# Performance work log

Measured on AMD Instinct MI355X. Metric: run time of the kernel, lower is better.

Reference implementation:

```python
import jax, jax.numpy as jnp
import numpy as np

T, B, D, Hd = 512, 64, 1024, 1024
SIGMA = 0.01


def setup_inputs() -> dict:
    key = jax.random.key(0)
    ks = jax.random.split(key, 9)
    inp = {
        "inputs": jax.random.normal(ks[0], (T, B, D), dtype=jnp.float32),
        "H0": jnp.zeros((B, Hd), dtype=jnp.float32),
        "C0": jnp.zeros((B, Hd), dtype=jnp.float32),
    }
    names_x = ["W_xi", "W_xf", "W_xo", "W_xc"]
    names_h = ["W_hi", "W_hf", "W_ho", "W_hc"]
    for i, n in enumerate(names_x):
        inp[n] = jax.random.normal(ks[1 + i], (D, Hd), dtype=jnp.float32) * SIGMA
    for i, n in enumerate(names_h):
        inp[n] = jax.random.normal(ks[5 + i], (Hd, Hd), dtype=jnp.float32) * SIGMA
    for n in ["b_i", "b_f", "b_o", "b_c"]:
        inp[n] = jnp.zeros((Hd,), dtype=jnp.float32)
    return inp


def reference(inputs, H0, C0, W_xi, W_xf, W_xo, W_xc,
              W_hi, W_hf, W_ho, W_hc, b_i, b_f, b_o, b_c):
    # Fuse the 4 input-projection and 4 hidden-projection GEMMs into 2 GEMMs
    # per step (same math as 8 separate matmuls, just concatenated).
    Wx = jnp.concatenate([W_xi, W_xf, W_xo, W_xc], axis=1)   # [D, 4H]
    Wh = jnp.concatenate([W_hi, W_hf, W_ho, W_hc], axis=1)   # [H, 4H]
    b = jnp.concatenate([b_i, b_f, b_o, b_c], axis=0)        # [4H]
    nh = b_i.shape[0]

    def step(carry, X):
        H, C = carry
        gates = X @ Wx + H @ Wh + b                          # [B, 4H]
        i, f, o, g = jnp.split(gates, 4, axis=1)
        I = jax.nn.sigmoid(i)
        F = jax.nn.sigmoid(f)
        O = jax.nn.sigmoid(o)
        C_tilde = jnp.tanh(g)
        C_new = F * C + I * C_tilde
        H_new = O * jnp.tanh(C_new)
        return (H_new, C_new), H_new

    (H_f, C_f), outputs = jax.lax.scan(step, (H0, C0), inputs)  # outputs [T, B, H]
    return outputs, (H_f, C_f)
```

## Files before the change

kernel.cpp:

```cpp
#include <hip/hip_runtime.h>
#include <cstdint>

#define TT 512
#define BB 64
#define DD 1024
#define HH 1024
#define NWG 128

typedef __attribute__((ext_vector_type(8))) __bf16 bf16x8;
typedef __attribute__((ext_vector_type(4))) float f32x4;

#define WS_XQ    0
#define WS_WHB   67108864ULL
#define WS_HQ    83886080ULL
#define WS_FLAGS 151126016ULL
#define FLAGS_BYTES ((TT + 1) * NWG * 4)

__device__ __forceinline__ unsigned short f2bf(float f) {
    unsigned int u = __float_as_uint(f);
    u = (u + 0x7fffu + ((u >> 16) & 1u)) >> 16;
    return (unsigned short)u;
}

__device__ __forceinline__ float sigm(float x) {
    return 1.0f / (1.0f + __expf(-x));
}
__device__ __forceinline__ float tanh_f(float x) {
    float a = fabsf(x);
    float e = __expf(-2.0f * a);
    float t = (1.0f - e) / (1.0f + e);
    return copysignf(t, x);
}

__device__ __forceinline__ unsigned long long pack4bf(float a, float b, float c, float d) {
    return (unsigned long long)f2bf(a)
         | ((unsigned long long)f2bf(b) << 16)
         | ((unsigned long long)f2bf(c) << 32)
         | ((unsigned long long)f2bf(d) << 48);
}

__global__ void cvt_x(const float* __restrict__ X, unsigned short* __restrict__ Xq) {
    int i = blockIdx.x * blockDim.x + threadIdx.x;
    const int n8 = TT * BB * DD / 8;
    if (i >= n8) return;
    const float4* s = (const float4*)X;
    float4 a = s[2 * i], b = s[2 * i + 1];
    union { unsigned short u[8]; uint4 q; } r;
    r.u[0] = f2bf(a.x); r.u[1] = f2bf(a.y); r.u[2] = f2bf(a.z); r.u[3] = f2bf(a.w);
    r.u[4] = f2bf(b.x); r.u[5] = f2bf(b.y); r.u[6] = f2bf(b.z); r.u[7] = f2bf(b.w);
    ((uint4*)Xq)[i] = r.q;
}

__global__ void pack_w(const float* __restrict__ Wxi, const float* __restrict__ Wxf,
                       const float* __restrict__ Wxo, const float* __restrict__ Wxc,
                       const float* __restrict__ Whi, const float* __restrict__ Whf,
                       const float* __restrict__ Who, const float* __restrict__ Whc,
                       unsigned short* __restrict__ WhB) {
    int tid = blockIdx.x * blockDim.x + threadIdx.x;
    int lane = tid & 63;
    int ct   = (tid >> 6) & 1;
    int s    = (tid >> 7) & 15;
    int kq   = (tid >> 11) & 3;
    int wg   = tid >> 13;
    int col  = ct * 16 + (lane & 15);
    int gate = col >> 3;
    int h    = wg * 8 + (col & 7);
    int kb   = kq * 512 + s * 32 + ((lane >> 4) & 3) * 8;

    const float* Wx[4] = {Wxi, Wxf, Wxo, Wxc};
    const float* Wh[4] = {Whi, Whf, Who, Whc};
    const float* W = (kb < 1024) ? (Wx[gate] + (size_t)kb * HH + h)
                                 : (Wh[gate] + (size_t)(kb - 1024) * HH + h);
    union { unsigned short u[8]; uint4 q; } r;
#pragma unroll
    for (int m = 0; m < 8; ++m) r.u[m] = f2bf(W[(size_t)m * HH]);
    *(uint4*)(WhB + (size_t)tid * 8) = r.q;
}

__global__ void __launch_bounds__(512, 2)
lstm_seq(const unsigned short* __restrict__ Xq, const unsigned short* __restrict__ WhB,
         unsigned short* __restrict__ Hq, int* flags,
         const float* __restrict__ H0, const float* __restrict__ C0,
         const float* __restrict__ bi, const float* __restrict__ bfp,
         const float* __restrict__ bo, const float* __restrict__ bc,
         float* __restrict__ out) {
    __shared__ float gpart[4][64][36];
    __shared__ float htile[64][8];

    const int wg    = blockIdx.x;
    const int tid   = threadIdx.x;
    const int wv    = tid >> 6;
    const int lane  = tid & 63;
    const int quad  = lane >> 4;
    const int l15   = lane & 15;
    const int rhalf = wv & 1;
    const int kq    = wv >> 1;
    const int arow0 = rhalf * 32 + l15;

    const int arow = tid >> 3;
    const int hh   = tid & 7;
    const int hcol = wg * 8 + hh;
    const float Bi = bi[hcol], Bf = bfp[hcol], Bo = bo[hcol], Bc = bc[hcol];
    float Cr = C0[(size_t)arow * HH + hcol];

    bf16x8 Breg[16][2];
    {
        const unsigned short* wp = WhB + (size_t)(wg * 4 + kq) * (16 * 2 * 64 * 8);
#pragma unroll
        for (int s = 0; s < 16; ++s)
#pragma unroll
            for (int ct = 0; ct < 2; ++ct)
                Breg[s][ct] = *(const bf16x8*)(wp + ((s * 2 + ct) * 64 + lane) * 8);
    }

    if (tid < 64) {
        const float* s = H0 + (size_t)tid * HH + wg * 8;
        unsigned long long a = pack4bf(s[0], s[1], s[2], s[3]);
        unsigned long long b = pack4bf(s[4], s[5], s[6], s[7]);
        unsigned long long* d = (unsigned long long*)(Hq + (size_t)tid * HH + wg * 8);
        __hip_atomic_store(d,     a, __ATOMIC_RELAXED, __HIP_MEMORY_SCOPE_AGENT);
        __hip_atomic_store(d + 1, b, __ATOMIC_RELAXED, __HIP_MEMORY_SCOPE_AGENT);
    }
    __syncthreads();
    if (tid == 0)
        __hip_atomic_store(&flags[wg], 1, __ATOMIC_RELAXED, __HIP_MEMORY_SCOPE_AGENT);

    for (int t = 0; t < TT; ++t) {
        f32x4 a00 = {0.f,0.f,0.f,0.f}, a01 = {0.f,0.f,0.f,0.f};
        f32x4 a10 = {0.f,0.f,0.f,0.f}, a11 = {0.f,0.f,0.f,0.f};

        if (kq < 2) {
            const unsigned short* xb = Xq + ((size_t)(t * BB + arow0)) * DD + kq * 512 + quad * 8;
#pragma unroll
            for (int s = 0; s < 16; ++s) {
                bf16x8 af0 = *(const bf16x8*)(xb + s * 32);
                bf16x8 af1 = *(const bf16x8*)(xb + 16 * DD + s * 32);
                a00 = __builtin_amdgcn_mfma_f32_16x16x32_bf16(af0, Breg[s][0], a00, 0, 0, 0);
                a01 = __builtin_amdgcn_mfma_f32_16x16x32_bf16(af0, Breg[s][1], a01, 0, 0, 0);
                a10 = __builtin_amdgcn_mfma_f32_16x16x32_bf16(af1, Breg[s][0], a10, 0, 0, 0);
                a11 = __builtin_amdgcn_mfma_f32_16x16x32_bf16(af1, Breg[s][1], a11, 0, 0, 0);
            }
        } else {
            const int* fp = flags + (size_t)t * NWG + (kq - 2) * 64 + lane;
            while (__hip_atomic_load(fp, __ATOMIC_RELAXED, __HIP_MEMORY_SCOPE_AGENT) == 0)
                __builtin_amdgcn_s_sleep(1);
            const unsigned short* hb = Hq + ((size_t)(t * BB + arow0)) * HH + (kq - 2) * 512 + quad * 8;
#pragma unroll
            for (int s = 0; s < 16; ++s) {
                bf16x8 af0 = *(const bf16x8*)(hb + s * 32);
                bf16x8 af1 = *(const bf16x8*)(hb + 16 * HH + s * 32);
                a00 = __builtin_amdgcn_mfma_f32_16x16x32_bf16(af0, Breg[s][0], a00, 0, 0, 0);
                a01 = __builtin_amdgcn_mfma_f32_16x16x32_bf16(af0, Breg[s][1], a01, 0, 0, 0);
                a10 = __builtin_amdgcn_mfma_f32_16x16x32_bf16(af1, Breg[s][0], a10, 0, 0, 0);
                a11 = __builtin_amdgcn_mfma_f32_16x16x32_bf16(af1, Breg[s][1], a11, 0, 0, 0);
            }
        }

#pragma unroll
        for (int r = 0; r < 4; ++r) {
            int row0 = rhalf * 32 + quad * 4 + r;
            gpart[kq][row0][l15]           = a00[r];
            gpart[kq][row0][16 + l15]      = a01[r];
            gpart[kq][row0 + 16][l15]      = a10[r];
            gpart[kq][row0 + 16][16 + l15] = a11[r];
        }
        __syncthreads();

        {
            float gi = gpart[0][arow][hh]      + gpart[1][arow][hh]
                     + gpart[2][arow][hh]      + gpart[3][arow][hh]      + Bi;
            float gf = gpart[0][arow][8 + hh]  + gpart[1][arow][8 + hh]
                     + gpart[2][arow][8 + hh]  + gpart[3][arow][8 + hh]  + Bf;
            float go = gpart[0][arow][16 + hh] + gpart[1][arow][16 + hh]
                     + gpart[2][arow][16 + hh] + gpart[3][arow][16 + hh] + Bo;
            float gc = gpart[0][arow][24 + hh] + gpart[1][arow][24 + hh]
                     + gpart[2][arow][24 + hh] + gpart[3][arow][24 + hh] + Bc;
            float I = sigm(gi), F = sigm(gf), O = sigm(go), G = tanh_f(gc);
            Cr = F * Cr + I * G;
            htile[arow][hh] = O * tanh_f(Cr);
        }
        __syncthreads();

        if (tid < 128) {
            int r2 = tid >> 1, half = tid & 1;
            float4 v = *(const float4*)&htile[r2][half * 4];
            *(float4*)(out + ((size_t)t * BB + r2) * HH + wg * 8 + half * 4) = v;
            unsigned long long pk = pack4bf(v.x, v.y, v.z, v.w);
            __hip_atomic_store(
                (unsigned long long*)(Hq + ((size_t)(t + 1) * BB + r2) * HH + wg * 8 + half * 4),
                pk, __ATOMIC_RELAXED, __HIP_MEMORY_SCOPE_AGENT);
            if (t == TT - 1) {
                *(float4*)(out + (size_t)TT * BB * HH + (size_t)r2 * HH + wg * 8 + half * 4) = v;
            }
        }
        __syncthreads();
        if (tid == 0)
            __hip_atomic_store(flags + (size_t)(t + 1) * NWG + wg, 1,
                               __ATOMIC_RELAXED, __HIP_MEMORY_SCOPE_AGENT);
    }

    float* cf = out + (size_t)TT * BB * HH + (size_t)BB * HH;
    cf[(size_t)arow * HH + hcol] = Cr;
}

extern "C" void kernel_launch(void* const* d_in, const int* in_sizes, int n_in,
                              void* d_out, int out_size, void* d_ws, size_t ws_size,
                              hipStream_t stream) {
    const float* X   = (const float*)d_in[0];
    const float* H0  = (const float*)d_in[1];
    const float* C0  = (const float*)d_in[2];
    const float* Wxi = (const float*)d_in[3];
    const float* Wxf = (const float*)d_in[4];
    const float* Wxo = (const float*)d_in[5];
    const float* Wxc = (const float*)d_in[6];
    const float* Whi = (const float*)d_in[7];
    const float* Whf = (const float*)d_in[8];
    const float* Who = (const float*)d_in[9];
    const float* Whc = (const float*)d_in[10];
    const float* bi  = (const float*)d_in[11];
    const float* bf_ = (const float*)d_in[12];
    const float* bo  = (const float*)d_in[13];
    const float* bc  = (const float*)d_in[14];

    char* ws = (char*)d_ws;
    unsigned short* Xq  = (unsigned short*)(ws + WS_XQ);
    unsigned short* WhB = (unsigned short*)(ws + WS_WHB);
    unsigned short* Hq  = (unsigned short*)(ws + WS_HQ);
    int* flags          = (int*)(ws + WS_FLAGS);

    hipMemsetAsync(flags, 0, FLAGS_BYTES, stream);

    hipLaunchKernelGGL(cvt_x, dim3(TT * BB * DD / 8 / 256), dim3(256), 0, stream, X, Xq);
    hipLaunchKernelGGL(pack_w, dim3(4096), dim3(256), 0, stream,
                       Wxi, Wxf, Wxo, Wxc, Whi, Whf, Who, Whc, WhB);
    hipLaunchKernelGGL(lstm_seq, dim3(NWG), dim3(512), 0, stream,
                       Xq, WhB, Hq, flags, H0, C0, bi, bf_, bo, bc, (float*)d_out);
}
```

Baseline: 5.592 ms.

## Split H-wait into halves, fuse activation with H publish, drop a barrier

The H-projection waves now wait on producer flags with a wave-wide ballot in two halves. They start MFMAs on the first half of H as soon as those 64 workgroups have published, then wait for the rest. The gate activation moves onto two waves that each compute four columns per row and write H and the outputs directly. A shared counter lets the second finishing wave raise the step flag, which removes the htile staging buffer and one __syncthreads per step. The gpart row stride is padded to 37 to cut LDS bank conflicts. The changes shorten the serial critical path of each recurrent step, at the cost of concentrating activation work on 128 threads and relying on the vmcnt wait plus relaxed atomics for ordering.

```diff
diff --git a/kernel.cpp b/kernel.cpp
--- a/kernel.cpp
+++ b/kernel.cpp
@@ -84,8 +84,8 @@
          const float* __restrict__ bi, const float* __restrict__ bfp,
          const float* __restrict__ bo, const float* __restrict__ bc,
          float* __restrict__ out) {
-    __shared__ float gpart[4][64][36];
-    __shared__ float htile[64][8];
+    __shared__ float gpart[4][64][37];
+    __shared__ int hs;
 
     const int wg    = blockIdx.x;
     const int tid   = threadIdx.x;
@@ -94,14 +94,27 @@
     const int quad  = lane >> 4;
     const int l15   = lane & 15;
     const int rhalf = wv & 1;
-    const int kq    = wv >> 1;
+    const bool isH  = (wv >= 4);
+    const int kq    = isH ? 2 + ((wv - 4) >> 1) : (wv >> 1);
     const int arow0 = rhalf * 32 + l15;
 
-    const int arow = tid >> 3;
-    const int hh   = tid & 7;
-    const int hcol = wg * 8 + hh;
-    const float Bi = bi[hcol], Bf = bfp[hcol], Bo = bo[hcol], Bc = bc[hcol];
-    float Cr = C0[(size_t)arow * HH + hcol];
+    const bool isAct = (wv == 4) || (wv == 5);
+    const int aidx   = tid - 256;
+    const int r2     = aidx >> 1;
+    const int ahalf  = aidx & 1;
+    const int hcol0  = wg * 8 + ahalf * 4;
+
+    float Bi[4], Bf[4], Bo[4], Bc[4], Cr[4];
+    if (isAct) {
+#pragma unroll
+        for (int j = 0; j < 4; ++j) {
+            Bi[j] = bi[hcol0 + j];
+            Bf[j] = bfp[hcol0 + j];
+            Bo[j] = bo[hcol0 + j];
+            Bc[j] = bc[hcol0 + j];
+            Cr[j] = C0[(size_t)r2 * HH + hcol0 + j];
+        }
+    }
 
     bf16x8 Breg[16][2];
     {
@@ -113,6 +126,7 @@
                 Breg[s][ct] = *(const bf16x8*)(wp + ((s * 2 + ct) * 64 + lane) * 8);
     }
 
+    if (tid == 0) hs = 0;
     if (tid < 64) {
         const float* s = H0 + (size_t)tid * HH + wg * 8;
         unsigned long long a = pack4bf(s[0], s[1], s[2], s[3]);
@@ -129,7 +143,7 @@
         f32x4 a00 = {0.f,0.f,0.f,0.f}, a01 = {0.f,0.f,0.f,0.f};
         f32x4 a10 = {0.f,0.f,0.f,0.f}, a11 = {0.f,0.f,0.f,0.f};
 
-        if (kq < 2) {
+        if (!isH) {
             const unsigned short* xb = Xq + ((size_t)(t * BB + arow0)) * DD + kq * 512 + quad * 8;
 #pragma unroll
             for (int s = 0; s < 16; ++s) {
@@ -141,18 +155,49 @@
                 a11 = __builtin_amdgcn_mfma_f32_16x16x32_bf16(af1, Breg[s][1], a11, 0, 0, 0);
             }
         } else {
-            const int* fp = flags + (size_t)t * NWG + (kq - 2) * 64 + lane;
-            while (__hip_atomic_load(fp, __ATOMIC_RELAXED, __HIP_MEMORY_SCOPE_AGENT) == 0)
-                __builtin_amdgcn_s_sleep(1);
-            const unsigned short* hb = Hq + ((size_t)(t * BB + arow0)) * HH + (kq - 2) * 512 + quad * 8;
-#pragma unroll
-            for (int s = 0; s < 16; ++s) {
-                bf16x8 af0 = *(const bf16x8*)(hb + s * 32);
-                bf16x8 af1 = *(const bf16x8*)(hb + 16 * HH + s * 32);
-                a00 = __builtin_amdgcn_mfma_f32_16x16x32_bf16(af0, Breg[s][0], a00, 0, 0, 0);
-                a01 = __builtin_amdgcn_mfma_f32_16x16x32_bf16(af0, Breg[s][1], a01, 0, 0, 0);
-                a10 = __builtin_amdgcn_mfma_f32_16x16x32_bf16(af1, Breg[s][0], a10, 0, 0, 0);
-                a11 = __builtin_amdgcn_mfma_f32_16x16x32_bf16(af1, Breg[s][1], a11, 0, 0, 0);
+            const int kqh = kq - 2;
+            const int* fp = flags + (size_t)t * NWG + kqh * 64 + lane;
+            const unsigned short* hb = Hq + ((size_t)(t * BB + arow0)) * HH + kqh * 512 + quad * 8;
+            int myf = 0;
+            unsigned long long got = 0;
+
+            while ((got & 0xFFFFFFFFull) != 0xFFFFFFFFull) {
+                if (!myf) myf = __hip_atomic_load(fp, __ATOMIC_RELAXED, __HIP_MEMORY_SCOPE_AGENT);
+                got = __ballot(myf != 0);
+                if ((got & 0xFFFFFFFFull) != 0xFFFFFFFFull) __builtin_amdgcn_s_sleep(1);
+            }
+            asm volatile("" ::: "memory");
+            bf16x8 af[8][2];
+#pragma unroll
+            for (int s = 0; s < 8; ++s) {
+                af[s][0] = *(const bf16x8*)(hb + s * 32);
+                af[s][1] = *(const bf16x8*)(hb + 16 * HH + s * 32);
+            }
+#pragma unroll
+            for (int s = 0; s < 8; ++s) {
+                a00 = __builtin_amdgcn_mfma_f32_16x16x32_bf16(af[s][0], Breg[s][0], a00, 0, 0, 0);
+                a01 = __builtin_amdgcn_mfma_f32_16x16x32_bf16(af[s][0], Breg[s][1], a01, 0, 0, 0);
+                a10 = __builtin_amdgcn_mfma_f32_16x16x32_bf16(af[s][1], Breg[s][0], a10, 0, 0, 0);
+                a11 = __builtin_amdgcn_mfma_f32_16x16x32_bf16(af[s][1], Breg[s][1], a11, 0, 0, 0);
+            }
+
+            while (got != ~0ull) {
+                if (!myf) myf = __hip_atomic_load(fp, __ATOMIC_RELAXED, __HIP_MEMORY_SCOPE_AGENT);
+                got = __ballot(myf != 0);
+                if (got != ~0ull) __builtin_amdgcn_s_sleep(1);
+            }
+            asm volatile("" ::: "memory");
+#pragma unroll
+            for (int s = 0; s < 8; ++s) {
+                af[s][0] = *(const bf16x8*)(hb + (8 + s) * 32);
+                af[s][1] = *(const bf16x8*)(hb + 16 * HH + (8 + s) * 32);
+            }
+#pragma unroll
+            for (int s = 0; s < 8; ++s) {
+                a00 = __builtin_amdgcn_mfma_f32_16x16x32_bf16(af[s][0], Breg[8 + s][0], a00, 0, 0, 0);
+                a01 = __builtin_amdgcn_mfma_f32_16x16x32_bf16(af[s][0], Breg[8 + s][1], a01, 0, 0, 0);
+                a10 = __builtin_amdgcn_mfma_f32_16x16x32_bf16(af[s][1], Breg[8 + s][0], a10, 0, 0, 0);
+                a11 = __builtin_amdgcn_mfma_f32_16x16x32_bf16(af[s][1], Breg[8 + s][1], a11, 0, 0, 0);
             }
         }
 
@@ -166,41 +211,47 @@
         }
         __syncthreads();
 
-        {
-            float gi = gpart[0][arow][hh]      + gpart[1][arow][hh]
-                     + gpart[2][arow][hh]      + gpart[3][arow][hh]      + Bi;
-            float gf = gpart[0][arow][8 + hh]  + gpart[1][arow][8 + hh]
-                     + gpart[2][arow][8 + hh]  + gpart[3][arow][8 + hh]  + Bf;
-            float go = gpart[0][arow][16 + hh] + gpart[1][arow][16 + hh]
-                     + gpart[2][arow][16 + hh] + gpart[3][arow][16 + hh] + Bo;
-            float gc = gpart[0][arow][24 + hh] + gpart[1][arow][24 + hh]
-                     + gpart[2][arow][24 + hh] + gpart[3][arow][24 + hh] + Bc;
-            float I = sigm(gi), F = sigm(gf), O = sigm(go), G = tanh_f(gc);
-            Cr = F * Cr + I * G;
-            htile[arow][hh] = O * tanh_f(Cr);
+        if (isAct) {
+            float hv[4];
+#pragma unroll
+            for (int j = 0; j < 4; ++j) {
+                const int c = ahalf * 4 + j;
+                float gi = gpart[0][r2][c]      + gpart[1][r2][c]
+                         + gpart[2][r2][c]      + gpart[3][r2][c]      + Bi[j];
+                float gf = gpart[0][r2][8 + c]  + gpart[1][r2][8 + c]
+                         + gpart[2][r2][8 + c]  + gpart[3][r2][8 + c]  + Bf[j];
+                float go = gpart[0][r2][16 + c] + gpart[1][r2][16 + c]
+                         + gpart[2][r2][16 + c] + gpart[3][r2][16 + c] + Bo[j];
+                float gc = gpart[0][r2][24 + c] + gpart[1][r2][24 + c]
+                         + gpart[2][r2][24 + c] + gpart[3][r2][24 + c] + Bc[j];
+                float I = sigm(gi), F = sigm(gf), O = sigm(go), G = tanh_f(gc);
+                Cr[j] = F * Cr[j] + I * G;
+                hv[j] = O * tanh_f(Cr[j]);
+            }
+            unsigned long long pk = pack4bf(hv[0], hv[1], hv[2], hv[3]);
+            __hip_atomic_store(
+                (unsigned long long*)(Hq + ((size_t)(t + 1) * BB + r2) * HH + hcol0),
+                pk, __ATOMIC_RELAXED, __HIP_MEMORY_SCOPE_AGENT);
+            asm volatile("s_waitcnt vmcnt(0)" ::: "memory");
+            if (lane == 0) {
+                int prev = atomicAdd(&hs, 1);
+                if (prev & 1)
+                    __hip_atomic_store(flags + (size_t)(t + 1) * NWG + wg, 1,
+                                       __ATOMIC_RELAXED, __HIP_MEMORY_SCOPE_AGENT);
+            }
+            float4 v = make_float4(hv[0], hv[1], hv[2], hv[3]);
+            *(float4*)(out + ((size_t)t * BB + r2) * HH + hcol0) = v;
+            if (t == TT - 1) {
+                *(float4*)(out + (size_t)TT * BB * HH + (size_t)r2 * HH + hcol0) = v;
+            }
         }
         __syncthreads();
-
-        if (tid < 128) {
-            int r2 = tid >> 1, half = tid & 1;
-            float4 v = *(const float4*)&htile[r2][half * 4];
-            *(float4*)(out + ((size_t)t * BB + r2) * HH + wg * 8 + half * 4) = v;
-            unsigned long long pk = pack4bf(v.x, v.y, v.z, v.w);
-            __hip_atomic_store(
-                (unsigned long long*)(Hq + ((size_t)(t + 1) * BB + r2) * HH + wg * 8 + half * 4),
-                pk, __ATOMIC_RELAXED, __HIP_MEMORY_SCOPE_AGENT);
-            if (t == TT - 1) {
-                *(float4*)(out + (size_t)TT * BB * HH + (size_t)r2 * HH + wg * 8 + half * 4) = v;
-            }
-        }
-        __syncthreads();
-        if (tid == 0)
-            __hip_atomic_store(flags + (size_t)(t + 1) * NWG + wg, 1,
-                               __ATOMIC_RELAXED, __HIP_MEMORY_SCOPE_AGENT);
-    }
-
-    float* cf = out + (size_t)TT * BB * HH + (size_t)BB * HH;
-    cf[(size_t)arow * HH + hcol] = Cr;
+    }
+
+    if (isAct) {
+        float* cf = out + (size_t)TT * BB * HH + (size_t)BB * HH;
+        *(float4*)(cf + (size_t)r2 * HH + hcol0) = make_float4(Cr[0], Cr[1], Cr[2], Cr[3]);
+    }
 }
 
 extern "C" void kernel_launch(void* const* d_in, const int* in_sizes, int n_in,
```

Result: no change. 5.561 ms (-0.6%).
